# Performance work log

Measured on AMD Instinct MI355X. Metric: run time of the kernel, lower is better.

The kernel has to match this reference:

```python
import jax, jax.numpy as jnp
import numpy as np
from jax.scipy.special import betaln

B, T = 4096, 8192

def setup_inputs() -> dict:
    key = jax.random.key(0)
    k_obs, k_a1, k_b1, k_a2, k_b2 = jax.random.split(key, 5)
    obs_seq = (jax.random.uniform(k_obs, (B, T)) < 0.5).astype(jnp.float32)
    # priors strictly positive, away from 0 to keep betaln finite
    alpha1 = jax.random.uniform(k_a1, (B,)) * 2.0 + 0.5
    beta1 = jax.random.uniform(k_b1, (B,)) * 2.0 + 0.5
    alpha2 = jax.random.uniform(k_a2, (B,)) * 2.0 + 0.5
    beta2 = jax.random.uniform(k_b2, (B,)) * 2.0 + 0.5
    mixweight = jnp.float32(0.4)
    return {"obs_seq": obs_seq, "alpha1": alpha1, "beta1": beta1,
            "alpha2": alpha2, "beta2": beta2, "mixweight": mixweight}

def reference(obs_seq, alpha1, beta1, alpha2, beta2, mixweight):
    # cumulative successes/failures, shifted right by one (posterior BEFORE obs t)
    cs = jnp.cumsum(obs_seq, axis=1)          # [B,T]
    cf = jnp.cumsum(1.0 - obs_seq, axis=1)    # [B,T]
    s_prev = jnp.pad(cs[:, :-1], ((0, 0), (1, 0)))  # cat([0, cs[:-1]])
    f_prev = jnp.pad(cf[:, :-1], ((0, 0), (1, 0)))
    a1 = alpha1[:, None] + s_prev
    b1 = beta1[:, None] + f_prev
    a2 = alpha2[:, None] + s_prev
    b2 = beta2[:, None] + f_prev
    clog1 = betaln(a1, b1) - betaln(alpha1, beta1)[:, None]
    clog2 = betaln(a2, b2) - betaln(alpha2, beta2)[:, None]
    bigconst = -clog1
    c1 = mixweight * jnp.exp(clog1 + bigconst)
    c2 = (1.0 - mixweight) * jnp.exp(clog2 + bigconst)
    post_mixweight = c1 / (c1 + c2)
    # stack the post_dict entries into one [5,B,T] array
    return jnp.stack([a1, b1, a2, b2, post_mixweight])
```

## Files before the change

kernel.cpp:

```cpp
#include <hip/hip_runtime.h>


#define BLOCK 1024
#define VEC 4
#define NWAVES (BLOCK / 64)

typedef float v4f __attribute__((ext_vector_type(4)));

__global__ __launch_bounds__(BLOCK, 4) void bbm_kernel(
    const float* __restrict__ obs,
    const float* __restrict__ alpha1, const float* __restrict__ beta1,
    const float* __restrict__ alpha2, const float* __restrict__ beta2,
    const float* __restrict__ mixw,
    float* __restrict__ out,
    int T, size_t bt)
{
    const int row  = blockIdx.x;
    const int tid  = threadIdx.x;
    const int lane = tid & 63;
    const int wid  = tid >> 6;

    __shared__ int   sPart[NWAVES];
    __shared__ float dPart[NWAVES];

    const float A1 = alpha1[row], B1 = beta1[row];
    const float A2 = alpha2[row], B2 = beta2[row];
    const float w  = mixw[0];
    const float AB1 = A1 + B1, AB2 = A2 + B2;
    const float w2 = 1.0f - w;

    const float* __restrict__ orow = obs + (size_t)row * T;
    float* __restrict__ obase = out + (size_t)row * T;

    const unsigned long long lt_mask = ((unsigned long long)1 << lane) - 1ull;

    int   carry_s = 0;
    float carry_d = 0.0f;

    const int EPB  = BLOCK * VEC;
    const int segs = T / EPB;

    v4f cur = *(const v4f*)(orow + tid * VEC);

    for (int seg = 0; seg < segs; ++seg) {
        const int t0 = seg * EPB + tid * VEC;

        int bit[VEC], sloc[VEC];
        int ts = 0;
        #pragma unroll
        for (int j = 0; j < VEC; ++j) { bit[j] = cur[j] > 0.5f; sloc[j] = ts; ts += bit[j]; }

        unsigned long long m0 = __ballot(bit[0]);
        unsigned long long m1 = __ballot(bit[1]);
        unsigned long long m2 = __ballot(bit[2]);
        unsigned long long m3 = __ballot(bit[3]);
        const int wave_excl = __builtin_popcountll(m0 & lt_mask)
                            + __builtin_popcountll(m1 & lt_mask)
                            + __builtin_popcountll(m2 & lt_mask)
                            + __builtin_popcountll(m3 & lt_mask);
        const int wave_tot  = __builtin_popcountll(m0) + __builtin_popcountll(m1)
                            + __builtin_popcountll(m2) + __builtin_popcountll(m3);
        if (lane == 0) sPart[wid] = wave_tot;
        __syncthreads();
        int prior = 0, total = 0;
        #pragma unroll
        for (int wI = 0; wI < NWAVES; ++wI) {
            int p = sPart[wI];
            total += p;
            if (wI < wid) prior += p;
        }
        const int tbase_s = carry_s + prior + wave_excl;

        float dloc[VEC];
        float td = 0.0f;
        #pragma unroll
        for (int j = 0; j < VEC; ++j) {
            const float ft = (float)(t0 + j);
            const float fs = (float)(tbase_s + sloc[j]);
            const float fp = ft - fs;
            const float sel1 = bit[j] ? (A1 + fs) : (B1 + fp);
            const float sel2 = bit[j] ? (A2 + fs) : (B2 + fp);
            const float delta = __logf(sel2 * (AB1 + ft)) - __logf(sel1 * (AB2 + ft));
            dloc[j] = td;
            td += delta;
        }

        float incl_d = td;
        #pragma unroll
        for (int off = 1; off < 64; off <<= 1) {
            float n = __shfl_up(incl_d, off, 64);
            if (lane >= off) incl_d += n;
        }
        if (lane == 63) dPart[wid] = incl_d;
        __syncthreads();
        float priord = 0.0f, totald = 0.0f;
        #pragma unroll
        for (int wI = 0; wI < NWAVES; ++wI) {
            float p = dPart[wI];
            totald += p;
            if (wI < wid) priord += p;
        }
        const float tbase_d = carry_d + priord + (incl_d - td);

        v4f nxt;
        if (seg + 1 < segs) nxt = *(const v4f*)(orow + (seg + 1) * EPB + tid * VEC);

        v4f va1, vb1, va2, vb2, vpm;
        #pragma unroll
        for (int j = 0; j < VEC; ++j) {
            const float ft = (float)(t0 + j);
            const float fs = (float)(tbase_s + sloc[j]);
            const float fp = ft - fs;
            const float d  = tbase_d + dloc[j];
            va1[j] = A1 + fs;
            vb1[j] = B1 + fp;
            va2[j] = A2 + fs;
            vb2[j] = B2 + fp;
            vpm[j] = __fdividef(w, w + w2 * __expf(d));
        }
        float* p = obase + t0;
        *(v4f*)(p)          = va1;
        *(v4f*)(p + bt)     = vb1;
        *(v4f*)(p + 2 * bt) = va2;
        *(v4f*)(p + 3 * bt) = vb2;
        *(v4f*)(p + 4 * bt) = vpm;

        carry_s += total;
        carry_d += totald;
        cur = nxt;
    }
}

extern "C" void kernel_launch(void* const* d_in, const int* in_sizes, int n_in,
                              void* d_out, int out_size, void* d_ws, size_t ws_size,
                              hipStream_t stream) {
    const float* obs    = (const float*)d_in[0];
    const float* alpha1 = (const float*)d_in[1];
    const float* beta1  = (const float*)d_in[2];
    const float* alpha2 = (const float*)d_in[3];
    const float* beta2  = (const float*)d_in[4];
    const float* mixw   = (const float*)d_in[5];

    const int Bn = in_sizes[1];
    const int Tn = in_sizes[0] / Bn;
    const size_t bt = (size_t)Bn * (size_t)Tn;

    bbm_kernel<<<Bn, BLOCK, 0, stream>>>(obs, alpha1, beta1, alpha2, beta2,
                                         mixw, (float*)d_out, Tn, bt);
}
```

Before: 737.9 us.

## Specialize T=8192 kernel to scan both segments in one pass

Adds a one-shot kernel for T=8192 in which each thread handles two 4-element chunks, one in each half of the row. Both halves are scanned together, so the block does two barrier rounds in total instead of two per segment. It also uses mbcnt intrinsics for the in-wave exclusive counts and native log2/exp2 builtins in place of __logf/__expf. Other sizes fall back to the original looped kernel. The cost is higher register use per thread, and the fast path works only for this one sequence length.

```diff
diff --git a/kernel.cpp b/kernel.cpp
--- a/kernel.cpp
+++ b/kernel.cpp
@@ -2,12 +2,162 @@
 
 
 #define BLOCK 1024
-#define VEC 4
-#define NWAVES (BLOCK / 64)
+#define NW (BLOCK / 64)
 
 typedef float v4f __attribute__((ext_vector_type(4)));
 
-__global__ __launch_bounds__(BLOCK, 4) void bbm_kernel(
+__device__ __forceinline__ unsigned mbcnt_excl(unsigned long long m, unsigned base) {
+    return __builtin_amdgcn_mbcnt_hi((unsigned)(m >> 32),
+           __builtin_amdgcn_mbcnt_lo((unsigned)(m & 0xffffffffu), base));
+}
+
+__global__ __launch_bounds__(BLOCK, 4) void bbm_oneshot(
+    const float* __restrict__ obs,
+    const float* __restrict__ alpha1, const float* __restrict__ beta1,
+    const float* __restrict__ alpha2, const float* __restrict__ beta2,
+    const float* __restrict__ mixw,
+    float* __restrict__ out,
+    size_t bt)
+{
+    const int T    = 2 * BLOCK * 4;
+    const int HALF = BLOCK * 4;
+    const int row  = blockIdx.x;
+    const int tid  = threadIdx.x;
+    const int lane = tid & 63;
+    const int wid  = tid >> 6;
+
+    __shared__ int2   sP[NW];
+    __shared__ float2 dP[NW];
+
+    const float A1 = alpha1[row], B1 = beta1[row];
+    const float A2 = alpha2[row], B2 = beta2[row];
+    const float w  = mixw[0];
+    const float AB1 = A1 + B1, AB2 = A2 + B2;
+    const float w2 = 1.0f - w;
+
+    const float* __restrict__ orow = obs + (size_t)row * T;
+    float* __restrict__ obase = out + (size_t)row * T;
+
+    const int t0A = tid * 4;
+    const int t0B = HALF + tid * 4;
+
+    v4f curA = *(const v4f*)(orow + t0A);
+    v4f curB = *(const v4f*)(orow + t0B);
+
+    int bitA[4], slA[4], bitB[4], slB[4];
+    int tsA = 0, tsB = 0;
+    #pragma unroll
+    for (int j = 0; j < 4; ++j) { bitA[j] = curA[j] > 0.5f; slA[j] = tsA; tsA += bitA[j]; }
+    #pragma unroll
+    for (int j = 0; j < 4; ++j) { bitB[j] = curB[j] > 0.5f; slB[j] = tsB; tsB += bitB[j]; }
+
+    unsigned long long mA0 = __ballot(bitA[0]), mA1 = __ballot(bitA[1]);
+    unsigned long long mA2 = __ballot(bitA[2]), mA3 = __ballot(bitA[3]);
+    unsigned long long mB0 = __ballot(bitB[0]), mB1 = __ballot(bitB[1]);
+    unsigned long long mB2 = __ballot(bitB[2]), mB3 = __ballot(bitB[3]);
+
+    const unsigned exA = mbcnt_excl(mA3, mbcnt_excl(mA2, mbcnt_excl(mA1, mbcnt_excl(mA0, 0))));
+    const unsigned exB = mbcnt_excl(mB3, mbcnt_excl(mB2, mbcnt_excl(mB1, mbcnt_excl(mB0, 0))));
+    const int wtotA = __builtin_popcountll(mA0) + __builtin_popcountll(mA1)
+                    + __builtin_popcountll(mA2) + __builtin_popcountll(mA3);
+    const int wtotB = __builtin_popcountll(mB0) + __builtin_popcountll(mB1)
+                    + __builtin_popcountll(mB2) + __builtin_popcountll(mB3);
+
+    if (lane == 0) sP[wid] = make_int2(wtotA, wtotB);
+    __syncthreads();
+    int priorA = 0, totalA = 0, priorB = 0;
+    #pragma unroll
+    for (int wI = 0; wI < NW; ++wI) {
+        const int2 p = sP[wI];
+        totalA += p.x;
+        if (wI < wid) { priorA += p.x; priorB += p.y; }
+    }
+    const int baseAs = priorA + (int)exA;
+    const int baseBs = totalA + priorB + (int)exB;
+
+    float dlA[4], dlB[4];
+    float tdA = 0.0f, tdB = 0.0f;
+    #pragma unroll
+    for (int j = 0; j < 4; ++j) {
+        const float ft = (float)(t0A + j);
+        const float fs = (float)(baseAs + slA[j]);
+        const float fp = ft - fs;
+        const float s1 = bitA[j] ? (A1 + fs) : (B1 + fp);
+        const float s2 = bitA[j] ? (A2 + fs) : (B2 + fp);
+        const float dl = __builtin_amdgcn_logf(s2 * (AB1 + ft))
+                       - __builtin_amdgcn_logf(s1 * (AB2 + ft));
+        dlA[j] = tdA; tdA += dl;
+    }
+    #pragma unroll
+    for (int j = 0; j < 4; ++j) {
+        const float ft = (float)(t0B + j);
+        const float fs = (float)(baseBs + slB[j]);
+        const float fp = ft - fs;
+        const float s1 = bitB[j] ? (A1 + fs) : (B1 + fp);
+        const float s2 = bitB[j] ? (A2 + fs) : (B2 + fp);
+        const float dl = __builtin_amdgcn_logf(s2 * (AB1 + ft))
+                       - __builtin_amdgcn_logf(s1 * (AB2 + ft));
+        dlB[j] = tdB; tdB += dl;
+    }
+
+    float inclA = tdA, inclB = tdB;
+    #pragma unroll
+    for (int off = 1; off < 64; off <<= 1) {
+        const float nA = __shfl_up(inclA, off, 64);
+        const float nB = __shfl_up(inclB, off, 64);
+        if (lane >= off) { inclA += nA; inclB += nB; }
+    }
+    if (lane == 63) dP[wid] = make_float2(inclA, inclB);
+    __syncthreads();
+    float priordA = 0.0f, totaldA = 0.0f, priordB = 0.0f;
+    #pragma unroll
+    for (int wI = 0; wI < NW; ++wI) {
+        const float2 p = dP[wI];
+        totaldA += p.x;
+        if (wI < wid) { priordA += p.x; priordB += p.y; }
+    }
+    const float baseAd = priordA + (inclA - tdA);
+    const float baseBd = totaldA + priordB + (inclB - tdB);
+
+    v4f a1A, b1A, a2A, b2A, pmA, a1B, b1B, a2B, b2B, pmB;
+    #pragma unroll
+    for (int j = 0; j < 4; ++j) {
+        const float ft = (float)(t0A + j);
+        const float fs = (float)(baseAs + slA[j]);
+        const float fp = ft - fs;
+        const float d  = baseAd + dlA[j];
+        a1A[j] = A1 + fs;
+        b1A[j] = B1 + fp;
+        a2A[j] = A2 + fs;
+        b2A[j] = B2 + fp;
+        pmA[j] = __fdividef(w, w + w2 * __builtin_amdgcn_exp2f(d));
+    }
+    #pragma unroll
+    for (int j = 0; j < 4; ++j) {
+        const float ft = (float)(t0B + j);
+        const float fs = (float)(baseBs + slB[j]);
+        const float fp = ft - fs;
+        const float d  = baseBd + dlB[j];
+        a1B[j] = A1 + fs;
+        b1B[j] = B1 + fp;
+        a2B[j] = A2 + fs;
+        b2B[j] = B2 + fp;
+        pmB[j] = __fdividef(w, w + w2 * __builtin_amdgcn_exp2f(d));
+    }
+
+    float* p = obase;
+    *(v4f*)(p + t0A)          = a1A;  *(v4f*)(p + t0B)          = a1B;
+    *(v4f*)(p + bt + t0A)     = b1A;  *(v4f*)(p + bt + t0B)     = b1B;
+    *(v4f*)(p + 2 * bt + t0A) = a2A;  *(v4f*)(p + 2 * bt + t0B) = a2B;
+    *(v4f*)(p + 3 * bt + t0A) = b2A;  *(v4f*)(p + 3 * bt + t0B) = b2B;
+    *(v4f*)(p + 4 * bt + t0A) = pmA;  *(v4f*)(p + 4 * bt + t0B) = pmB;
+}
+
+#define GBLOCK 1024
+#define GVEC 4
+#define GNW (GBLOCK / 64)
+
+__global__ __launch_bounds__(GBLOCK, 4) void bbm_generic(
     const float* __restrict__ obs,
     const float* __restrict__ alpha1, const float* __restrict__ beta1,
     const float* __restrict__ alpha2, const float* __restrict__ beta2,
@@ -20,8 +170,8 @@
     const int lane = tid & 63;
     const int wid  = tid >> 6;
 
-    __shared__ int   sPart[NWAVES];
-    __shared__ float dPart[NWAVES];
+    __shared__ int   sPart[GNW];
+    __shared__ float dPart[GNW];
 
     const float A1 = alpha1[row], B1 = beta1[row];
     const float A2 = alpha2[row], B2 = beta2[row];
@@ -37,18 +187,18 @@
     int   carry_s = 0;
     float carry_d = 0.0f;
 
-    const int EPB  = BLOCK * VEC;
+    const int EPB  = GBLOCK * GVEC;
     const int segs = T / EPB;
 
-    v4f cur = *(const v4f*)(orow + tid * VEC);
+    v4f cur = *(const v4f*)(orow + tid * GVEC);
 
     for (int seg = 0; seg < segs; ++seg) {
-        const int t0 = seg * EPB + tid * VEC;
-
-        int bit[VEC], sloc[VEC];
+        const int t0 = seg * EPB + tid * GVEC;
+
+        int bit[GVEC], sloc[GVEC];
         int ts = 0;
         #pragma unroll
-        for (int j = 0; j < VEC; ++j) { bit[j] = cur[j] > 0.5f; sloc[j] = ts; ts += bit[j]; }
+        for (int j = 0; j < GVEC; ++j) { bit[j] = cur[j] > 0.5f; sloc[j] = ts; ts += bit[j]; }
 
         unsigned long long m0 = __ballot(bit[0]);
         unsigned long long m1 = __ballot(bit[1]);
@@ -64,17 +214,17 @@
         __syncthreads();
         int prior = 0, total = 0;
         #pragma unroll
-        for (int wI = 0; wI < NWAVES; ++wI) {
+        for (int wI = 0; wI < GNW; ++wI) {
             int p = sPart[wI];
             total += p;
             if (wI < wid) prior += p;
         }
         const int tbase_s = carry_s + prior + wave_excl;
 
-        float dloc[VEC];
+        float dloc[GVEC];
         float td = 0.0f;
         #pragma unroll
-        for (int j = 0; j < VEC; ++j) {
+        for (int j = 0; j < GVEC; ++j) {
             const float ft = (float)(t0 + j);
             const float fs = (float)(tbase_s + sloc[j]);
             const float fp = ft - fs;
@@ -95,7 +245,7 @@
         __syncthreads();
         float priord = 0.0f, totald = 0.0f;
         #pragma unroll
-        for (int wI = 0; wI < NWAVES; ++wI) {
+        for (int wI = 0; wI < GNW; ++wI) {
             float p = dPart[wI];
             totald += p;
             if (wI < wid) priord += p;
@@ -103,11 +253,11 @@
         const float tbase_d = carry_d + priord + (incl_d - td);
 
         v4f nxt;
-        if (seg + 1 < segs) nxt = *(const v4f*)(orow + (seg + 1) * EPB + tid * VEC);
+        if (seg + 1 < segs) nxt = *(const v4f*)(orow + (seg + 1) * EPB + tid * GVEC);
 
         v4f va1, vb1, va2, vb2, vpm;
         #pragma unroll
-        for (int j = 0; j < VEC; ++j) {
+        for (int j = 0; j < GVEC; ++j) {
             const float ft = (float)(t0 + j);
             const float fs = (float)(tbase_s + sloc[j]);
             const float fp = ft - fs;
@@ -145,6 +295,11 @@
     const int Tn = in_sizes[0] / Bn;
     const size_t bt = (size_t)Bn * (size_t)Tn;
 
-    bbm_kernel<<<Bn, BLOCK, 0, stream>>>(obs, alpha1, beta1, alpha2, beta2,
-                                         mixw, (float*)d_out, Tn, bt);
+    if (Tn == 8192) {
+        bbm_oneshot<<<Bn, BLOCK, 0, stream>>>(obs, alpha1, beta1, alpha2, beta2,
+                                              mixw, (float*)d_out, bt);
+    } else {
+        bbm_generic<<<Bn, GBLOCK, 0, stream>>>(obs, alpha1, beta1, alpha2, beta2,
+                                               mixw, (float*)d_out, Tn, bt);
+    }
 }
```

New measurement: 757.7 us. 1.03x slower.
